# Kernel optimization log

Measured on AMD Instinct MI355X. Metric: run time of the kernel, lower is better.

## Reference

```python
import jax, jax.numpy as jnp
import numpy as np

# Grid / problem sizes (full-res grid for sp_tensor_1; sp_tensor_2 lives on the half-res grid
# and its indices are multiplied by 2 in forward, so they land on even full-res coords).
B, Z, Y, X = 2, 21, 400, 352
Z2, Y2, X2 = 11, 200, 176
N1, N2 = 160000, 60000
CIN, COUT = 64, 128
EPS = 1e-3  # BatchNorm eps


def _build_rulebook():
    """Precompute the SubMConv3d rulebook (spconv builds this once per indice_key).
    Returns padded gather/scatter index arrays for the 26 non-center taps and N.
    Padding uses index N (a dummy zero row / dropped output row)."""
    rng = np.random.default_rng(0)
    # sp_tensor_2: unique voxels on half-res grid, coords scaled by 2 (as done in forward)
    lin2 = rng.choice(B * Z2 * Y2 * X2, size=N2, replace=False)
    b2 = lin2 // (Z2 * Y2 * X2); r = lin2 % (Z2 * Y2 * X2)
    z2 = r // (Y2 * X2); r = r % (Y2 * X2); y2 = r // X2; x2 = r % X2
    c2 = np.stack([b2, 2 * z2, 2 * y2, 2 * x2], 1).astype(np.int64)
    key2 = ((c2[:, 0] * Z + c2[:, 1]) * Y + c2[:, 2]) * X + c2[:, 3]
    # sp_tensor_1: unique voxels on full-res grid, disjoint from scaled sp2 voxels
    lin1 = rng.choice(B * Z * Y * X, size=N1 + 20000, replace=False)
    lin1 = lin1[~np.isin(lin1, key2)][:N1].astype(np.int64)
    b1 = lin1 // (Z * Y * X); r = lin1 % (Z * Y * X)
    z1 = r // (Y * X); r = r % (Y * X); y1 = r // X; x1 = r % X
    c1 = np.stack([b1, z1, y1, x1], 1)
    coords = np.concatenate([c1, c2], 0)  # [N,4] -- sp1 rows first, matching feature concat
    N = coords.shape[0]
    keys = ((coords[:, 0] * Z + coords[:, 1]) * Y + coords[:, 2]) * X + coords[:, 3]
    order = np.argsort(keys); skeys = keys[order]
    gathers, scatters = [], []
    for dz in (-1, 0, 1):
        for dy in (-1, 0, 1):
            for dx in (-1, 0, 1):
                if dz == 0 and dy == 0 and dx == 0:
                    continue  # center tap handled as a dense identity-indexed GEMM
                q = coords[:, 1:] + np.array([dz, dy, dx])
                valid = (q >= 0).all(1) & (q[:, 0] < Z) & (q[:, 1] < Y) & (q[:, 2] < X)
                qk = ((coords[:, 0] * Z + q[:, 0]) * Y + q[:, 1]) * X + q[:, 2]
                pos = np.clip(np.searchsorted(skeys, qk), 0, N - 1)
                hit = valid & (skeys[pos] == qk)
                gathers.append(order[pos[hit]])
                scatters.append(np.nonzero(hit)[0])
    Pmax = max(len(g) for g in gathers)
    G = np.full((26, Pmax), N, np.int32)
    S = np.full((26, Pmax), N, np.int32)
    for i, (g, s) in enumerate(zip(gathers, scatters)):
        G[i, :len(g)] = g
        S[i, :len(s)] = s
    return G, S, N


def setup_inputs() -> dict:
    G, S, N = _build_rulebook()
    k1, k2, k3, k4 = jax.random.split(jax.random.key(0), 4)
    return {
        "features1": jax.random.normal(k1, (N1, CIN), jnp.float32),
        "features2": jax.random.normal(k2, (N - N1, CIN), jnp.float32),
        "weight": jax.random.normal(k3, (27, CIN, COUT), jnp.float32) * (1.0 / np.sqrt(27 * CIN)),
        "bias": jax.random.normal(k4, (COUT,), jnp.float32) * 0.01,
        "gamma": jnp.ones((COUT,), jnp.float32),
        "beta": jnp.zeros((COUT,), jnp.float32),
        "gather_idx": jnp.asarray(G),
        "scatter_idx": jnp.asarray(S),
    }


def reference(features1, features2, weight, bias, gamma, beta, gather_idx, scatter_idx):
    # forward(): concat features of both sparse tensors along the voxel axis
    feats = jnp.concatenate([features1, features2], axis=0)  # [N, Cin]
    N = feats.shape[0]
    # SubMConv3d via gather-GEMM-scatter over the precomputed rulebook.
    # Center tap (kernel index 13): every output voxel pairs with itself -> dense GEMM.
    out = feats @ weight[13] + bias  # [N, Cout]
    # dummy row N absorbs padded rulebook entries
    out = jnp.concatenate([out, jnp.zeros((1, out.shape[1]), out.dtype)], axis=0)
    feats_pad = jnp.concatenate([feats, jnp.zeros((1, feats.shape[1]), feats.dtype)], axis=0)
    taps = [k for k in range(27) if k != 13]
    for i, k in enumerate(taps):
        msg = feats_pad[gather_idx[i]] @ weight[k]  # [Pmax, Cout]
        out = out.at[scatter_idx[i]].add(msg)
    out = out[:N]
    # BatchNorm1d (training mode: batch statistics, biased variance) + ReLU
    mean = jnp.mean(out, axis=0)
    var = jnp.var(out, axis=0)
    out = (out - mean) * jax.lax.rsqrt(var + EPS) * gamma + beta
    return jax.nn.relu(out)
```

## Files before the change

kernel.cpp:

```cpp
#include <hip/hip_runtime.h>

#define EPS 1e-3f

typedef __attribute__((ext_vector_type(8))) short bf8_t;
typedef __attribute__((ext_vector_type(4))) float f32x4;

static __device__ __forceinline__ unsigned f2bf_pack(float a, float b) {
  union { float f; unsigned u; } ca, cb;
  ca.f = a; cb.f = b;
  unsigned ra = (ca.u + 0x7FFFu + ((ca.u >> 16) & 1u)) >> 16;
  unsigned rb = (cb.u + 0x7FFFu + ((cb.u >> 16) & 1u)) >> 16;
  return ra | (rb << 16);
}
static __device__ __forceinline__ unsigned short f2bf1(float x) {
  union { float f; unsigned u; } c; c.f = x;
  return (unsigned short)((c.u + 0x7FFFu + ((c.u >> 16) & 1u)) >> 16);
}
static __device__ __forceinline__ float bf2f(unsigned bits16) {
  union { unsigned u; float f; } c;
  c.u = bits16 << 16;
  return c.f;
}


__global__ __launch_bounds__(256) void to_bf16(
    const float* __restrict__ f1, const float* __restrict__ f2,
    unsigned short* __restrict__ fbuf, int N1, int N) {
  int idx = blockIdx.x * 256 + threadIdx.x;
  if (idx >= (N + 1) * 8) return;
  int row = idx >> 3, seg = idx & 7;
  uint4 o = make_uint4(0, 0, 0, 0);
  if (row < N) {
    const float* src = (row < N1) ? (f1 + (size_t)row * 64)
                                  : (f2 + (size_t)(row - N1) * 64);
    float4 v0 = *(const float4*)(src + seg * 8);
    float4 v1 = *(const float4*)(src + seg * 8 + 4);
    o.x = f2bf_pack(v0.x, v0.y); o.y = f2bf_pack(v0.z, v0.w);
    o.z = f2bf_pack(v1.x, v1.y); o.w = f2bf_pack(v1.z, v1.w);
  }
  *(uint4*)(fbuf + (size_t)idx * 8) = o;
}

__global__ __launch_bounds__(256) void wconv(
    const float* __restrict__ W, unsigned short* __restrict__ Wb) {
  int idx = blockIdx.x * 256 + threadIdx.x;
  int k = idx & 63, n = (idx >> 6) & 127, t = idx >> 13;
  Wb[idx] = f2bf1(W[((size_t)t * 64 + k) * 128 + n]);
}

__global__ __launch_bounds__(256) void count_slots(
    const int* __restrict__ S, unsigned char* __restrict__ SL,
    int* __restrict__ cnt, int N, int pm) {
  const int p = blockIdx.x * 256 + threadIdx.x;
  const int i = blockIdx.y;
  if (p >= pm) return;
  const int idx = i * pm + p;
  const int s = S[idx];
  if (s < N) SL[idx] = (unsigned char)atomicAdd(&cnt[s], 1);
}

__global__ __launch_bounds__(256) void prefix_base(
    const int* __restrict__ cnt, int2* __restrict__ BC,
    int* __restrict__ gtot, int N) {
  const int t = threadIdx.x;
  const int j0 = blockIdx.x * 1024 + t * 4;
  int c0 = 0, c1 = 0, c2 = 0, c3 = 0;
  if (j0 + 3 < N) {
    int4 c = *(const int4*)(cnt + j0);
    c0 = c.x; c1 = c.y; c2 = c.z; c3 = c.w;
  } else {
    if (j0 < N) c0 = cnt[j0];
    if (j0 + 1 < N) c1 = cnt[j0 + 1];
    if (j0 + 2 < N) c2 = cnt[j0 + 2];
  }
  const int tsum = c0 + c1 + c2 + c3;
  int incl = tsum;
#pragma unroll
  for (int off = 1; off < 64; off <<= 1) {
    int u = __shfl_up(incl, off, 64);
    if ((t & 63) >= off) incl += u;
  }
  __shared__ int wsum[4];
  if ((t & 63) == 63) wsum[t >> 6] = incl;
  __syncthreads();
  if (t == 0) {
    int w0 = wsum[0], w1 = wsum[1], w2 = wsum[2], w3 = wsum[3];
    int gb = atomicAdd(gtot, w0 + w1 + w2 + w3);
    wsum[0] = gb; wsum[1] = gb + w0;
    wsum[2] = gb + w0 + w1; wsum[3] = gb + w0 + w1 + w2;
  }
  __syncthreads();
  const int excl = wsum[t >> 6] + incl - tsum;
  if (j0 < N) BC[j0] = make_int2(excl, c0);
  if (j0 + 1 < N) BC[j0 + 1] = make_int2(excl + c0, c1);
  if (j0 + 2 < N) BC[j0 + 2] = make_int2(excl + c0 + c1, c2);
  if (j0 + 3 < N) BC[j0 + 3] = make_int2(excl + c0 + c1 + c2, c3);
}

__global__ __launch_bounds__(256) void center_mfma(
    const unsigned short* __restrict__ fbuf,
    const unsigned short* __restrict__ Wb13,
    const float* __restrict__ bias,
    unsigned short* __restrict__ outb, int N) {
  __shared__ unsigned short A[128 * 64];
  const int tid = threadIdx.x;
  const int row0 = blockIdx.x * 128;

#pragma unroll
  for (int it = 0; it < 4; ++it) {
    int flat = it * 256 + tid;
    int r = flat >> 3, qs = flat & 7;
    int g = row0 + r; if (g >= N) g = N;
    uint4 v = *(const uint4*)(fbuf + (size_t)g * 64 + qs * 8);
    int rt = r >> 4, m = r & 15, c = qs >> 2, qq = qs & 3;
    *(uint4*)(A + ((rt * 2 + c) * 64 + qq * 16 + m) * 8) = v;
  }
  __syncthreads();

  const int wave = tid >> 6, lane = tid & 63;
  const int ncol = lane & 15, q2 = lane >> 4;
  bf8_t Bf[2][2];
  float bs[2];
#pragma unroll
  for (int ct = 0; ct < 2; ++ct) {
    int col = wave * 32 + ct * 16 + ncol;
    bs[ct] = bias[col];
#pragma unroll
    for (int c = 0; c < 2; ++c)
      Bf[ct][c] = *(const bf8_t*)(Wb13 + (size_t)col * 64 + c * 32 + q2 * 8);
  }
  f32x4 acc[8][2];
#pragma unroll
  for (int rt = 0; rt < 8; ++rt)
#pragma unroll
    for (int ct = 0; ct < 2; ++ct) acc[rt][ct] = (f32x4){0.f, 0.f, 0.f, 0.f};

#pragma unroll
  for (int rt = 0; rt < 8; ++rt) {
    bf8_t a0 = *(const bf8_t*)(A + ((rt * 2 + 0) * 64 + lane) * 8);
    bf8_t a1 = *(const bf8_t*)(A + ((rt * 2 + 1) * 64 + lane) * 8);
#pragma unroll
    for (int ct = 0; ct < 2; ++ct) {
      acc[rt][ct] = __builtin_amdgcn_mfma_f32_16x16x32_bf16(a0, Bf[ct][0], acc[rt][ct], 0, 0, 0);
      acc[rt][ct] = __builtin_amdgcn_mfma_f32_16x16x32_bf16(a1, Bf[ct][1], acc[rt][ct], 0, 0, 0);
    }
  }

#pragma unroll
  for (int rt = 0; rt < 8; ++rt)
#pragma unroll
    for (int ct = 0; ct < 2; ++ct) {
      int col = wave * 32 + ct * 16 + ncol;
#pragma unroll
      for (int e = 0; e < 4; ++e) {
        int row = row0 + rt * 16 + q2 * 4 + e;
        if (row < N)
          outb[(size_t)row * 128 + col] = f2bf1(acc[rt][ct][e] + bs[ct]);
      }
    }
}

__global__ __launch_bounds__(256) void msg_mfma_c(
    const unsigned short* __restrict__ fbuf,
    const unsigned short* __restrict__ Wb,
    const int* __restrict__ G, const int* __restrict__ S,
    const int2* __restrict__ BC, const unsigned char* __restrict__ SL,
    unsigned short* __restrict__ compact, int N, int pm) {
  const int tap = blockIdx.y;
  const int ktap = tap + (tap >= 13 ? 1 : 0);
  const unsigned short* Wt = Wb + (size_t)ktap * 128 * 64;
  const int* Gi = G + (size_t)tap * pm;
  const int* Si = S + (size_t)tap * pm;
  const int p0 = blockIdx.x * 128;
  if (Gi[p0] >= N) return;

  __shared__ unsigned short A[128 * 64];
  __shared__ int g_lds[128];
  __shared__ int d_lds[128];
  const int tid = threadIdx.x;
  if (tid < 128) {
    int p = p0 + tid;
    int g = N, d = -1;
    if (p < pm) {
      g = Gi[p];
      int s = Si[p];
      if (s < N) d = BC[s].x + (int)SL[(size_t)tap * pm + p];
    }
    g_lds[tid] = g;
    d_lds[tid] = d;
  }
  __syncthreads();

#pragma unroll
  for (int it = 0; it < 4; ++it) {
    int flat = it * 256 + tid;
    int r = flat >> 3, qs = flat & 7;
    int g = g_lds[r];
    uint4 v = *(const uint4*)(fbuf + (size_t)g * 64 + qs * 8);
    int rt = r >> 4, m = r & 15, c = qs >> 2, qq = qs & 3;
    *(uint4*)(A + ((rt * 2 + c) * 64 + qq * 16 + m) * 8) = v;
  }
  __syncthreads();

  const int wave = tid >> 6, lane = tid & 63;
  const int ncol = lane & 15, q2 = lane >> 4;
  bf8_t Bf[2][2];
#pragma unroll
  for (int ct = 0; ct < 2; ++ct) {
    int col = wave * 32 + ct * 16 + ncol;
#pragma unroll
    for (int c = 0; c < 2; ++c)
      Bf[ct][c] = *(const bf8_t*)(Wt + (size_t)col * 64 + c * 32 + q2 * 8);
  }
  f32x4 acc[8][2];
#pragma unroll
  for (int rt = 0; rt < 8; ++rt)
#pragma unroll
    for (int ct = 0; ct < 2; ++ct) acc[rt][ct] = (f32x4){0.f, 0.f, 0.f, 0.f};

#pragma unroll
  for (int rt = 0; rt < 8; ++rt) {
    bf8_t a0 = *(const bf8_t*)(A + ((rt * 2 + 0) * 64 + lane) * 8);
    bf8_t a1 = *(const bf8_t*)(A + ((rt * 2 + 1) * 64 + lane) * 8);
#pragma unroll
    for (int ct = 0; ct < 2; ++ct) {
      acc[rt][ct] = __builtin_amdgcn_mfma_f32_16x16x32_bf16(a0, Bf[ct][0], acc[rt][ct], 0, 0, 0);
      acc[rt][ct] = __builtin_amdgcn_mfma_f32_16x16x32_bf16(a1, Bf[ct][1], acc[rt][ct], 0, 0, 0);
    }
  }

#pragma unroll
  for (int rt = 0; rt < 8; ++rt) {
    int dl[4];
#pragma unroll
    for (int e = 0; e < 4; ++e) dl[e] = d_lds[rt * 16 + q2 * 4 + e];
#pragma unroll
    for (int ct = 0; ct < 2; ++ct) {
      int col = wave * 32 + ct * 16 + ncol;
#pragma unroll
      for (int e = 0; e < 4; ++e)
        if (dl[e] >= 0)
          compact[(size_t)dl[e] * 128 + col] = f2bf1(acc[rt][ct][e]);
    }
  }
}

__global__ __launch_bounds__(256) void combine_c(
    unsigned short* __restrict__ outb, const int2* __restrict__ BC,
    const unsigned short* __restrict__ compact, float* __restrict__ ws,
    int N) {
  const int tid = threadIdx.x;
  const int grp = tid >> 5, l = tid & 31;
  float4 s = make_float4(0.f, 0.f, 0.f, 0.f);
  float4 q = make_float4(0.f, 0.f, 0.f, 0.f);

  for (int j = blockIdx.x * 8 + grp; j < N; j += gridDim.x * 8) {
    int2 bc = BC[j];
    uint2 ov = ((const uint2*)(outb + (size_t)j * 128))[l];
    float4 v;
    v.x = bf2f(ov.x & 0xffffu); v.y = bf2f(ov.x >> 16);
    v.z = bf2f(ov.y & 0xffffu); v.w = bf2f(ov.y >> 16);
    for (int k = 0; k < bc.y; ++k) {
      uint2 mv = ((const uint2*)(compact + (size_t)(bc.x + k) * 128))[l];
      v.x += bf2f(mv.x & 0xffffu); v.y += bf2f(mv.x >> 16);
      v.z += bf2f(mv.y & 0xffffu); v.w += bf2f(mv.y >> 16);
    }
    if (bc.y) {
      uint2 pk;
      pk.x = f2bf_pack(v.x, v.y); pk.y = f2bf_pack(v.z, v.w);
      ((uint2*)(outb + (size_t)j * 128))[l] = pk;
    }
    s.x += v.x; s.y += v.y; s.z += v.z; s.w += v.w;
    q.x += v.x * v.x; q.y += v.y * v.y; q.z += v.z * v.z; q.w += v.w * v.w;
  }

  __shared__ float red[8 * 32 * 9];
  float* my = red + (grp * 32 + l) * 9;
  my[0] = s.x; my[1] = s.y; my[2] = s.z; my[3] = s.w;
  my[4] = q.x; my[5] = q.y; my[6] = q.z; my[7] = q.w;
  __syncthreads();
  {
    int c4 = tid & 31, jj = tid >> 5;
    float v = 0.f;
#pragma unroll
    for (int g = 0; g < 8; ++g) v += red[(g * 32 + c4) * 9 + jj];
    int col = c4 * 4 + (jj & 3);
    unsafeAtomicAdd(&ws[(jj >> 2) * 4096 + col * 16], v);
  }
}

__global__ __launch_bounds__(256) void norm_b(
    const unsigned short* __restrict__ outb, float* __restrict__ out,
    const float* __restrict__ ws, const float* __restrict__ gamma,
    const float* __restrict__ beta, int total8, float invN) {
  const int tid0 = blockIdx.x * 256 + threadIdx.x;
  const int c0 = (tid0 & 15) * 8;
  float sc[8], sh[8];
#pragma unroll
  for (int k = 0; k < 8; ++k) {
    float m = ws[(c0 + k) * 16] * invN;
    float var = ws[4096 + (c0 + k) * 16] * invN - m * m;
    sc[k] = gamma[c0 + k] * rsqrtf(var + EPS);
    sh[k] = beta[c0 + k] - m * sc[k];
  }
  for (int idx = tid0; idx < total8; idx += gridDim.x * 256) {
    uint4 v = *(const uint4*)(outb + (size_t)idx * 8);
    float f0 = bf2f(v.x & 0xffffu), f1 = bf2f(v.x >> 16);
    float f2 = bf2f(v.y & 0xffffu), f3 = bf2f(v.y >> 16);
    float f4 = bf2f(v.z & 0xffffu), f5 = bf2f(v.z >> 16);
    float f6 = bf2f(v.w & 0xffffu), f7 = bf2f(v.w >> 16);
    float4 o0, o1;
    o0.x = fmaxf(f0 * sc[0] + sh[0], 0.f);
    o0.y = fmaxf(f1 * sc[1] + sh[1], 0.f);
    o0.z = fmaxf(f2 * sc[2] + sh[2], 0.f);
    o0.w = fmaxf(f3 * sc[3] + sh[3], 0.f);
    o1.x = fmaxf(f4 * sc[4] + sh[4], 0.f);
    o1.y = fmaxf(f5 * sc[5] + sh[5], 0.f);
    o1.z = fmaxf(f6 * sc[6] + sh[6], 0.f);
    o1.w = fmaxf(f7 * sc[7] + sh[7], 0.f);
    *(float4*)(out + (size_t)idx * 8) = o0;
    *(float4*)(out + (size_t)idx * 8 + 4) = o1;
  }
}


__global__ __launch_bounds__(256) void scatter_R(
    const int* __restrict__ S, int* __restrict__ R, int N, int pm) {
  const int p = blockIdx.x * 256 + threadIdx.x;
  const int i = blockIdx.y;
  if (p >= pm) return;
  const int idx = i * pm + p;
  const int s = S[idx];
  if (s < N) R[(size_t)s * 26 + i] = idx;
}

__global__ __launch_bounds__(256) void center_gemm(
    const float* __restrict__ f1, const float* __restrict__ f2,
    const float* __restrict__ W, const float* __restrict__ bias,
    float* __restrict__ out, int N, int N1) {
  __shared__ float fLDS[128 * 65];
  __shared__ float wLDS[32 * 128];
  const int tid = threadIdx.x;
  const int tx = tid & 15, ty = tid >> 4;
  const int row0 = blockIdx.x * 128;

  for (int k = 0; k < 8; ++k) {
    int flat4 = tid + k * 256;
    int row = flat4 >> 4, c4 = flat4 & 15;
    int grow = row0 + row;
    float4 v = make_float4(0.f, 0.f, 0.f, 0.f);
    if (grow < N) {
      const float* src = (grow < N1) ? (f1 + (size_t)grow * 64)
                                     : (f2 + (size_t)(grow - N1) * 64);
      v = *(const float4*)(src + c4 * 4);
    }
    int l = row * 65 + c4 * 4;
    fLDS[l + 0] = v.x; fLDS[l + 1] = v.y; fLDS[l + 2] = v.z; fLDS[l + 3] = v.w;
  }
  float acc[8][8];
#pragma unroll
  for (int r = 0; r < 8; ++r)
#pragma unroll
    for (int j = 0; j < 8; ++j) acc[r][j] = 0.f;
  for (int kk = 0; kk < 64; kk += 32) {
    __syncthreads();
    for (int k = 0; k < 4; ++k) {
      int flat4 = tid + k * 256;
      int c = flat4 >> 5, col4 = flat4 & 31;
      float4 v = *(const float4*)(W + (size_t)(kk + c) * 128 + col4 * 4);
      *(float4*)(wLDS + c * 128 + col4 * 4) = v;
    }
    __syncthreads();
#pragma unroll 4
    for (int c = 0; c < 32; ++c) {
      float a[8];
#pragma unroll
      for (int r = 0; r < 8; ++r) a[r] = fLDS[(ty * 8 + r) * 65 + kk + c];
      float4 b0 = *(const float4*)(wLDS + c * 128 + tx * 8);
      float4 b1 = *(const float4*)(wLDS + c * 128 + tx * 8 + 4);
      float b[8] = {b0.x, b0.y, b0.z, b0.w, b1.x, b1.y, b1.z, b1.w};
#pragma unroll
      for (int r = 0; r < 8; ++r)
#pragma unroll
        for (int j = 0; j < 8; ++j) acc[r][j] += a[r] * b[j];
    }
  }
  float4 bi0 = *(const float4*)(bias + tx * 8);
  float4 bi1 = *(const float4*)(bias + tx * 8 + 4);
#pragma unroll
  for (int r = 0; r < 8; ++r) {
    int grow = row0 + ty * 8 + r;
    if (grow < N) {
      float4 o0 = make_float4(acc[r][0] + bi0.x, acc[r][1] + bi0.y,
                              acc[r][2] + bi0.z, acc[r][3] + bi0.w);
      float4 o1 = make_float4(acc[r][4] + bi1.x, acc[r][5] + bi1.y,
                              acc[r][6] + bi1.z, acc[r][7] + bi1.w);
      float* dst = out + (size_t)grow * 128 + tx * 8;
      *(float4*)dst = o0;
      *(float4*)(dst + 4) = o1;
    }
  }
}

__global__ __launch_bounds__(256) void msg_gemm_buf(
    const float* __restrict__ f1, const float* __restrict__ f2,
    const float* __restrict__ W27, const int* __restrict__ G,
    const int* __restrict__ S, unsigned short* __restrict__ msgbuf,
    int N, int N1, int pm) {
  const int i = blockIdx.y;
  const int ktap = i + (i >= 13 ? 1 : 0);
  const float* W = W27 + (size_t)ktap * 64 * 128;
  const int* Gi = G + (size_t)i * pm;
  const int* Si = S + (size_t)i * pm;
  const int p0 = blockIdx.x * 128;
  if (Si[p0] >= N) return;
  __shared__ float fLDS[128 * 65];
  __shared__ float wLDS[32 * 128];
  const int tid = threadIdx.x;
  const int tx = tid & 15, ty = tid >> 4;
  for (int k = 0; k < 8; ++k) {
    int flat4 = tid + k * 256;
    int row = flat4 >> 4, c4 = flat4 & 15;
    int p = p0 + row;
    float4 v = make_float4(0.f, 0.f, 0.f, 0.f);
    if (p < pm) {
      int g = Gi[p];
      if (g < N) {
        const float* src = (g < N1) ? (f1 + (size_t)g * 64)
                                    : (f2 + (size_t)(g - N1) * 64);
        v = *(const float4*)(src + c4 * 4);
      }
    }
    int l = row * 65 + c4 * 4;
    fLDS[l + 0] = v.x; fLDS[l + 1] = v.y; fLDS[l + 2] = v.z; fLDS[l + 3] = v.w;
  }
  float acc[8][8];
#pragma unroll
  for (int r = 0; r < 8; ++r)
#pragma unroll
    for (int j = 0; j < 8; ++j) acc[r][j] = 0.f;
  for (int kk = 0; kk < 64; kk += 32) {
    __syncthreads();
    for (int k = 0; k < 4; ++k) {
      int flat4 = tid + k * 256;
      int c = flat4 >> 5, col4 = flat4 & 31;
      float4 v = *(const float4*)(W + (size_t)(kk + c) * 128 + col4 * 4);
      *(float4*)(wLDS + c * 128 + col4 * 4) = v;
    }
    __syncthreads();
#pragma unroll 4
    for (int c = 0; c < 32; ++c) {
      float a[8];
#pragma unroll
      for (int r = 0; r < 8; ++r) a[r] = fLDS[(ty * 8 + r) * 65 + kk + c];
      float4 b0 = *(const float4*)(wLDS + c * 128 + tx * 8);
      float4 b1 = *(const float4*)(wLDS + c * 128 + tx * 8 + 4);
      float b[8] = {b0.x, b0.y, b0.z, b0.w, b1.x, b1.y, b1.z, b1.w};
#pragma unroll
      for (int r = 0; r < 8; ++r)
#pragma unroll
        for (int j = 0; j < 8; ++j) acc[r][j] += a[r] * b[j];
    }
  }
#pragma unroll
  for (int r = 0; r < 8; ++r) {
    int p = p0 + ty * 8 + r;
    if (p < pm) {
      uint4 pk;
      pk.x = f2bf_pack(acc[r][0], acc[r][1]);
      pk.y = f2bf_pack(acc[r][2], acc[r][3]);
      pk.z = f2bf_pack(acc[r][4], acc[r][5]);
      pk.w = f2bf_pack(acc[r][6], acc[r][7]);
      *(uint4*)(msgbuf + ((size_t)i * pm + p) * 128 + tx * 8) = pk;
    }
  }
}

__global__ __launch_bounds__(256) void msg_gemm(
    const float* __restrict__ f1, const float* __restrict__ f2,
    const float* __restrict__ W27, const int* __restrict__ G,
    const int* __restrict__ S, float* __restrict__ out,
    int N, int N1, int pm) {
  const int i = blockIdx.y;
  const int ktap = i + (i >= 13 ? 1 : 0);
  const float* W = W27 + (size_t)ktap * 64 * 128;
  const int* Gi = G + (size_t)i * pm;
  const int* Si = S + (size_t)i * pm;
  const int p0 = blockIdx.x * 128;
  if (Si[p0] >= N) return;
  __shared__ float fLDS[128 * 65];
  __shared__ float wLDS[32 * 128];
  const int tid = threadIdx.x;
  const int tx = tid & 15, ty = tid >> 4;
  for (int k = 0; k < 8; ++k) {
    int flat4 = tid + k * 256;
    int row = flat4 >> 4, c4 = flat4 & 15;
    int p = p0 + row;
    float4 v = make_float4(0.f, 0.f, 0.f, 0.f);
    if (p < pm) {
      int g = Gi[p];
      if (g < N) {
        const float* src = (g < N1) ? (f1 + (size_t)g * 64)
                                    : (f2 + (size_t)(g - N1) * 64);
        v = *(const float4*)(src + c4 * 4);
      }
    }
    int l = row * 65 + c4 * 4;
    fLDS[l + 0] = v.x; fLDS[l + 1] = v.y; fLDS[l + 2] = v.z; fLDS[l + 3] = v.w;
  }
  float acc[8][8];
#pragma unroll
  for (int r = 0; r < 8; ++r)
#pragma unroll
    for (int j = 0; j < 8; ++j) acc[r][j] = 0.f;
  for (int kk = 0; kk < 64; kk += 32) {
    __syncthreads();
    for (int k = 0; k < 4; ++k) {
      int flat4 = tid + k * 256;
      int c = flat4 >> 5, col4 = flat4 & 31;
      float4 v = *(const float4*)(W + (size_t)(kk + c) * 128 + col4 * 4);
      *(float4*)(wLDS + c * 128 + col4 * 4) = v;
    }
    __syncthreads();
#pragma unroll 4
    for (int c = 0; c < 32; ++c) {
      float a[8];
#pragma unroll
      for (int r = 0; r < 8; ++r) a[r] = fLDS[(ty * 8 + r) * 65 + kk + c];
      float4 b0 = *(const float4*)(wLDS + c * 128 + tx * 8);
      float4 b1 = *(const float4*)(wLDS + c * 128 + tx * 8 + 4);
      float b[8] = {b0.x, b0.y, b0.z, b0.w, b1.x, b1.y, b1.z, b1.w};
#pragma unroll
      for (int r = 0; r < 8; ++r)
#pragma unroll
        for (int j = 0; j < 8; ++j) acc[r][j] += a[r] * b[j];
    }
  }
#pragma unroll
  for (int r = 0; r < 8; ++r) {
    int p = p0 + ty * 8 + r;
    if (p < pm) {
      int s = Si[p];
      if (s < N) {
        float* dst = out + (size_t)s * 128 + tx * 8;
#pragma unroll
        for (int j = 0; j < 8; ++j) unsafeAtomicAdd(dst + j, acc[r][j]);
      }
    }
  }
}

__global__ __launch_bounds__(256) void combine_stats(
    float* __restrict__ out, const int* __restrict__ R,
    const unsigned short* __restrict__ msgbuf, float* __restrict__ ws,
    int N) {
  const int tid = threadIdx.x;
  const int grp = tid >> 5, l = tid & 31;
  const int base = tid & 32;
  float4 s = make_float4(0.f, 0.f, 0.f, 0.f);
  float4 q = make_float4(0.f, 0.f, 0.f, 0.f);
  for (int j = blockIdx.x * 8 + grp; j < N; j += gridDim.x * 8) {
    float4 v = ((const float4*)(out + (size_t)j * 128))[l];
    int r = (l < 26) ? R[(size_t)j * 26 + l] : -1;
    unsigned long long bal = __ballot(r >= 0);
    unsigned mym = (unsigned)((bal >> base) & 0x3FFFFFFull);
    const bool any = (mym != 0);
    while (mym) {
      int b = __builtin_ctz(mym);
      mym &= mym - 1;
      int ptr = __shfl(r, base + b, 64);
      uint2 mv = ((const uint2*)(msgbuf + (size_t)ptr * 128))[l];
      v.x += bf2f(mv.x & 0xffffu);
      v.y += bf2f(mv.x >> 16);
      v.z += bf2f(mv.y & 0xffffu);
      v.w += bf2f(mv.y >> 16);
    }
    if (any) ((float4*)(out + (size_t)j * 128))[l] = v;
    s.x += v.x; s.y += v.y; s.z += v.z; s.w += v.w;
    q.x += v.x * v.x; q.y += v.y * v.y; q.z += v.z * v.z; q.w += v.w * v.w;
  }
  __shared__ float red[8 * 32 * 8];
  float* my = red + (grp * 32 + l) * 8;
  my[0] = s.x; my[1] = s.y; my[2] = s.z; my[3] = s.w;
  my[4] = q.x; my[5] = q.y; my[6] = q.z; my[7] = q.w;
  __syncthreads();
  {
    int c4 = tid & 31, j = tid >> 5;
    float v = 0.f;
#pragma unroll
    for (int g = 0; g < 8; ++g) v += red[(g * 32 + c4) * 8 + j];
    int col = c4 * 4 + (j & 3);
    unsafeAtomicAdd(&ws[col + (j >> 2) * 128], v);
  }
}

__global__ __launch_bounds__(256) void stats_kernel(
    const float* __restrict__ out, float* __restrict__ ws, int total4) {
  const int tid = threadIdx.x;
  float4 s = make_float4(0.f, 0.f, 0.f, 0.f);
  float4 q = make_float4(0.f, 0.f, 0.f, 0.f);
  const float4* o4 = (const float4*)out;
  for (int idx = blockIdx.x * 256 + tid; idx < total4; idx += gridDim.x * 256) {
    float4 v = o4[idx];
    s.x += v.x; s.y += v.y; s.z += v.z; s.w += v.w;
    q.x += v.x * v.x; q.y += v.y * v.y; q.z += v.z * v.z; q.w += v.w * v.w;
  }
  __shared__ float red[8 * 32 * 8];
  const int col4 = tid & 31, grpq = tid >> 5;
  float* my = red + (grpq * 32 + col4) * 8;
  my[0] = s.x; my[1] = s.y; my[2] = s.z; my[3] = s.w;
  my[4] = q.x; my[5] = q.y; my[6] = q.z; my[7] = q.w;
  __syncthreads();
  {
    int c4 = tid & 31, j = tid >> 5;
    float v = 0.f;
#pragma unroll
    for (int g = 0; g < 8; ++g) v += red[(g * 32 + c4) * 8 + j];
    int col = c4 * 4 + (j & 3);
    unsafeAtomicAdd(&ws[col + (j >> 2) * 128], v);
  }
}

__global__ __launch_bounds__(256) void norm_kernel(
    float* __restrict__ out, const float* __restrict__ ws,
    const float* __restrict__ gamma, const float* __restrict__ beta,
    int total4, float invN) {
  const int tid = threadIdx.x;
  const int c4 = tid & 31;
  float4 s = ((const float4*)ws)[c4];
  float4 q = ((const float4*)ws)[32 + c4];
  float4 g = ((const float4*)gamma)[c4];
  float4 b = ((const float4*)beta)[c4];
  float m0 = s.x * invN, m1 = s.y * invN, m2 = s.z * invN, m3 = s.w * invN;
  float sc0 = g.x * rsqrtf(q.x * invN - m0 * m0 + EPS);
  float sc1 = g.y * rsqrtf(q.y * invN - m1 * m1 + EPS);
  float sc2 = g.z * rsqrtf(q.z * invN - m2 * m2 + EPS);
  float sc3 = g.w * rsqrtf(q.w * invN - m3 * m3 + EPS);
  float sh0 = b.x - m0 * sc0, sh1 = b.y - m1 * sc1;
  float sh2 = b.z - m2 * sc2, sh3 = b.w - m3 * sc3;
  float4* o4 = (float4*)out;
  for (int idx = blockIdx.x * 256 + tid; idx < total4; idx += gridDim.x * 256) {
    float4 v = o4[idx];
    v.x = fmaxf(v.x * sc0 + sh0, 0.f);
    v.y = fmaxf(v.y * sc1 + sh1, 0.f);
    v.z = fmaxf(v.z * sc2 + sh2, 0.f);
    v.w = fmaxf(v.w * sc3 + sh3, 0.f);
    o4[idx] = v;
  }
}

extern "C" void kernel_launch(void* const* d_in, const int* in_sizes, int n_in,
                              void* d_out, int out_size, void* d_ws, size_t ws_size,
                              hipStream_t stream) {
  const float* f1 = (const float*)d_in[0];
  const float* f2 = (const float*)d_in[1];
  const float* W = (const float*)d_in[2];
  const float* bias = (const float*)d_in[3];
  const float* gamma = (const float*)d_in[4];
  const float* beta = (const float*)d_in[5];
  const int* G = (const int*)d_in[6];
  const int* S = (const int*)d_in[7];
  const int N1 = in_sizes[0] / 64;
  const int N2 = in_sizes[1] / 64;
  const int N = N1 + N2;
  const int pm = in_sizes[6] / 26;
  float* out = (float*)d_out;
  float* ws = (float*)d_ws;

  const size_t AL = 255;
  const size_t offC = 32768;
  const size_t Cb = (size_t)N * 4;
  const size_t offBC = (offC + Cb + AL) & ~AL;
  const size_t BCb = (size_t)N * 8;
  const size_t offSL = (offBC + BCb + AL) & ~AL;
  const size_t SLb = (size_t)26 * pm;
  const size_t offF = (offSL + SLb + AL) & ~AL;
  const size_t Fb = (size_t)(N + 1) * 64 * 2;
  const size_t offW = (offF + Fb + AL) & ~AL;
  const size_t Wbyt = (size_t)27 * 128 * 64 * 2;
  const size_t offM = (offW + Wbyt + AL) & ~AL;
  const size_t Mb = (size_t)26 * pm * 128 * 2;
  const size_t offO = (offM + Mb + AL) & ~AL;
  const size_t Ob = (size_t)N * 128 * 2;
  const bool full = ws_size >= offO + Ob;

  const size_t Rb = (size_t)N * 26 * 4;
  const size_t offR2 = 1024;
  const size_t offM2 = (offR2 + Rb + AL) & ~AL;
  const bool fast2 = ws_size >= offM2 + Mb;

  if (full) {
    int* cnt = (int*)((char*)d_ws + offC);
    int2* BC = (int2*)((char*)d_ws + offBC);
    unsigned char* SLp = (unsigned char*)((char*)d_ws + offSL);
    unsigned short* fbuf = (unsigned short*)((char*)d_ws + offF);
    unsigned short* Wb = (unsigned short*)((char*)d_ws + offW);
    unsigned short* compact = (unsigned short*)((char*)d_ws + offM);
    unsigned short* outb = (unsigned short*)((char*)d_ws + offO);
    int* gtot = (int*)((char*)d_ws + 28672);

    (void)hipMemsetAsync(ws, 0, 32768, stream);
    (void)hipMemsetAsync(cnt, 0, Cb, stream);
    to_bf16<<<((N + 1) * 8 + 255) / 256, 256, 0, stream>>>(f1, f2, fbuf, N1, N);
    wconv<<<(27 * 128 * 64) / 256, 256, 0, stream>>>(W, Wb);
    count_slots<<<dim3((pm + 255) / 256, 26), 256, 0, stream>>>(S, SLp, cnt, N, pm);
    prefix_base<<<(N + 1023) / 1024, 256, 0, stream>>>(cnt, BC, gtot, N);

    center_mfma<<<(N + 127) / 128, 256, 0, stream>>>(
        fbuf, Wb + (size_t)13 * 128 * 64, bias, outb, N);
    msg_mfma_c<<<dim3((pm + 127) / 128, 26), 256, 0, stream>>>(
        fbuf, Wb, G, S, BC, SLp, compact, N, pm);

    combine_c<<<2048, 256, 0, stream>>>(outb, BC, compact, ws, N);
    norm_b<<<2048, 256, 0, stream>>>(outb, out, ws, gamma, beta, N * 16,
                                     1.0f / N);
  } else if (fast2) {
    int* R = (int*)((char*)d_ws + offR2);
    unsigned short* msgbuf = (unsigned short*)((char*)d_ws + offM2);
    (void)hipMemsetAsync(ws, 0, 256 * sizeof(float), stream);
    (void)hipMemsetAsync(R, 0xFF, Rb, stream);
    center_gemm<<<(N + 127) / 128, 256, 0, stream>>>(
        f1, f2, W + (size_t)13 * 64 * 128, bias, out, N, N1);
    scatter_R<<<dim3((pm + 255) / 256, 26), 256, 0, stream>>>(S, R, N, pm);
    msg_gemm_buf<<<dim3((pm + 127) / 128, 26), 256, 0, stream>>>(
        f1, f2, W, G, S, msgbuf, N, N1, pm);
    combine_stats<<<1024, 256, 0, stream>>>(out, R, msgbuf, ws, N);
    norm_kernel<<<2048, 256, 0, stream>>>(out, ws, gamma, beta, N * 32,
                                          1.0f / N);
  } else {
    (void)hipMemsetAsync(ws, 0, 256 * sizeof(float), stream);
    center_gemm<<<(N + 127) / 128, 256, 0, stream>>>(
        f1, f2, W + (size_t)13 * 64 * 128, bias, out, N, N1);
    msg_gemm<<<dim3((pm + 127) / 128, 26), 256, 0, stream>>>(
        f1, f2, W, G, S, out, N, N1, pm);
    stats_kernel<<<1024, 256, 0, stream>>>(out, ws, N * 32);
    norm_kernel<<<2048, 256, 0, stream>>>(out, ws, gamma, beta, N * 32,
                                          1.0f / N);
  }
}
```

Baseline: 334.1 us.

## Fuse prep kernels and merge center GEMM into combine/stats pass

Merges the bf16 feature conversion, weight conversion and slot-counting kernels into one launch, and folds the two memsets into a single contiguous memset. Moves the center-tap MFMA GEMM into the combine kernel, so the center result stays in LDS and is summed with the compacted messages before the single write of outb. This removes one full round-trip of the bf16 output tensor plus several launch gaps. The combine kernel now uses 32KB of LDS and a fixed 128-row block tiling instead of a grid-stride loop, which may lower occupancy and load balance.

Result: faster. 297.1 us (-11.1%).

```diff
diff --git a/kernel.cpp b/kernel.cpp
--- a/kernel.cpp
+++ b/kernel.cpp
@@ -23,40 +23,41 @@
 }
 
 
-__global__ __launch_bounds__(256) void to_bf16(
+__global__ __launch_bounds__(256) void prep(
+    const float* __restrict__ W, unsigned short* __restrict__ Wb,
     const float* __restrict__ f1, const float* __restrict__ f2,
-    unsigned short* __restrict__ fbuf, int N1, int N) {
-  int idx = blockIdx.x * 256 + threadIdx.x;
-  if (idx >= (N + 1) * 8) return;
-  int row = idx >> 3, seg = idx & 7;
-  uint4 o = make_uint4(0, 0, 0, 0);
-  if (row < N) {
-    const float* src = (row < N1) ? (f1 + (size_t)row * 64)
-                                  : (f2 + (size_t)(row - N1) * 64);
-    float4 v0 = *(const float4*)(src + seg * 8);
-    float4 v1 = *(const float4*)(src + seg * 8 + 4);
-    o.x = f2bf_pack(v0.x, v0.y); o.y = f2bf_pack(v0.z, v0.w);
-    o.z = f2bf_pack(v1.x, v1.y); o.w = f2bf_pack(v1.z, v1.w);
-  }
-  *(uint4*)(fbuf + (size_t)idx * 8) = o;
-}
-
-__global__ __launch_bounds__(256) void wconv(
-    const float* __restrict__ W, unsigned short* __restrict__ Wb) {
-  int idx = blockIdx.x * 256 + threadIdx.x;
-  int k = idx & 63, n = (idx >> 6) & 127, t = idx >> 13;
-  Wb[idx] = f2bf1(W[((size_t)t * 64 + k) * 128 + n]);
-}
-
-__global__ __launch_bounds__(256) void count_slots(
+    unsigned short* __restrict__ fbuf,
     const int* __restrict__ S, unsigned char* __restrict__ SL,
-    int* __restrict__ cnt, int N, int pm) {
-  const int p = blockIdx.x * 256 + threadIdx.x;
-  const int i = blockIdx.y;
-  if (p >= pm) return;
-  const int idx = i * pm + p;
-  const int s = S[idx];
-  if (s < N) SL[idx] = (unsigned char)atomicAdd(&cnt[s], 1);
+    int* __restrict__ cnt, int N, int N1, int pm,
+    int wblocks, int fblocks, int cpb) {
+  const int bid = blockIdx.x;
+  if (bid < wblocks) {
+    int idx = bid * 256 + threadIdx.x;
+    int k = idx & 63, n = (idx >> 6) & 127, t = idx >> 13;
+    Wb[idx] = f2bf1(W[((size_t)t * 64 + k) * 128 + n]);
+  } else if (bid < wblocks + fblocks) {
+    int idx = (bid - wblocks) * 256 + threadIdx.x;
+    if (idx >= (N + 1) * 8) return;
+    int row = idx >> 3, seg = idx & 7;
+    uint4 o = make_uint4(0, 0, 0, 0);
+    if (row < N) {
+      const float* src = (row < N1) ? (f1 + (size_t)row * 64)
+                                    : (f2 + (size_t)(row - N1) * 64);
+      float4 v0 = *(const float4*)(src + seg * 8);
+      float4 v1 = *(const float4*)(src + seg * 8 + 4);
+      o.x = f2bf_pack(v0.x, v0.y); o.y = f2bf_pack(v0.z, v0.w);
+      o.z = f2bf_pack(v1.x, v1.y); o.w = f2bf_pack(v1.z, v1.w);
+    }
+    *(uint4*)(fbuf + (size_t)idx * 8) = o;
+  } else {
+    int b = bid - wblocks - fblocks;
+    int tap = b / cpb;
+    int p = (b - tap * cpb) * 256 + threadIdx.x;
+    if (p >= pm) return;
+    const int idx = tap * pm + p;
+    const int s = S[idx];
+    if (s < N) SL[idx] = (unsigned char)atomicAdd(&cnt[s], 1);
+  }
 }
 
 __global__ __launch_bounds__(256) void prefix_base(
@@ -97,69 +98,6 @@
   if (j0 + 3 < N) BC[j0 + 3] = make_int2(excl + c0 + c1 + c2, c3);
 }
 
-__global__ __launch_bounds__(256) void center_mfma(
-    const unsigned short* __restrict__ fbuf,
-    const unsigned short* __restrict__ Wb13,
-    const float* __restrict__ bias,
-    unsigned short* __restrict__ outb, int N) {
-  __shared__ unsigned short A[128 * 64];
-  const int tid = threadIdx.x;
-  const int row0 = blockIdx.x * 128;
-
-#pragma unroll
-  for (int it = 0; it < 4; ++it) {
-    int flat = it * 256 + tid;
-    int r = flat >> 3, qs = flat & 7;
-    int g = row0 + r; if (g >= N) g = N;
-    uint4 v = *(const uint4*)(fbuf + (size_t)g * 64 + qs * 8);
-    int rt = r >> 4, m = r & 15, c = qs >> 2, qq = qs & 3;
-    *(uint4*)(A + ((rt * 2 + c) * 64 + qq * 16 + m) * 8) = v;
-  }
-  __syncthreads();
-
-  const int wave = tid >> 6, lane = tid & 63;
-  const int ncol = lane & 15, q2 = lane >> 4;
-  bf8_t Bf[2][2];
-  float bs[2];
-#pragma unroll
-  for (int ct = 0; ct < 2; ++ct) {
-    int col = wave * 32 + ct * 16 + ncol;
-    bs[ct] = bias[col];
-#pragma unroll
-    for (int c = 0; c < 2; ++c)
-      Bf[ct][c] = *(const bf8_t*)(Wb13 + (size_t)col * 64 + c * 32 + q2 * 8);
-  }
-  f32x4 acc[8][2];
-#pragma unroll
-  for (int rt = 0; rt < 8; ++rt)
-#pragma unroll
-    for (int ct = 0; ct < 2; ++ct) acc[rt][ct] = (f32x4){0.f, 0.f, 0.f, 0.f};
-
-#pragma unroll
-  for (int rt = 0; rt < 8; ++rt) {
-    bf8_t a0 = *(const bf8_t*)(A + ((rt * 2 + 0) * 64 + lane) * 8);
-    bf8_t a1 = *(const bf8_t*)(A + ((rt * 2 + 1) * 64 + lane) * 8);
-#pragma unroll
-    for (int ct = 0; ct < 2; ++ct) {
-      acc[rt][ct] = __builtin_amdgcn_mfma_f32_16x16x32_bf16(a0, Bf[ct][0], acc[rt][ct], 0, 0, 0);
-      acc[rt][ct] = __builtin_amdgcn_mfma_f32_16x16x32_bf16(a1, Bf[ct][1], acc[rt][ct], 0, 0, 0);
-    }
-  }
-
-#pragma unroll
-  for (int rt = 0; rt < 8; ++rt)
-#pragma unroll
-    for (int ct = 0; ct < 2; ++ct) {
-      int col = wave * 32 + ct * 16 + ncol;
-#pragma unroll
-      for (int e = 0; e < 4; ++e) {
-        int row = row0 + rt * 16 + q2 * 4 + e;
-        if (row < N)
-          outb[(size_t)row * 128 + col] = f2bf1(acc[rt][ct][e] + bs[ct]);
-      }
-    }
-}
-
 __global__ __launch_bounds__(256) void msg_mfma_c(
     const unsigned short* __restrict__ fbuf,
     const unsigned short* __restrict__ Wb,
@@ -245,36 +183,100 @@
   }
 }
 
-__global__ __launch_bounds__(256) void combine_c(
-    unsigned short* __restrict__ outb, const int2* __restrict__ BC,
-    const unsigned short* __restrict__ compact, float* __restrict__ ws,
-    int N) {
+__global__ __launch_bounds__(256) void center_combine(
+    const unsigned short* __restrict__ fbuf,
+    const unsigned short* __restrict__ Wb13, const float* __restrict__ bias,
+    const int2* __restrict__ BC, const unsigned short* __restrict__ compact,
+    unsigned short* __restrict__ outb, float* __restrict__ ws, int N) {
+  __shared__ unsigned short SH[128 * 128];
+  __shared__ int2 bc_lds[128];
   const int tid = threadIdx.x;
+  const int row0 = blockIdx.x * 128;
+
+  if (tid < 128) {
+    int j = row0 + tid;
+    bc_lds[tid] = (j < N) ? BC[j] : make_int2(0, 0);
+  }
+
+#pragma unroll
+  for (int it = 0; it < 4; ++it) {
+    int flat = it * 256 + tid;
+    int r = flat >> 3, qs = flat & 7;
+    int g = row0 + r; if (g >= N) g = N;
+    uint4 v = *(const uint4*)(fbuf + (size_t)g * 64 + qs * 8);
+    int rt = r >> 4, m = r & 15, c = qs >> 2, qq = qs & 3;
+    *(uint4*)(SH + ((rt * 2 + c) * 64 + qq * 16 + m) * 8) = v;
+  }
+  __syncthreads();
+
+  const int wave = tid >> 6, lane = tid & 63;
+  const int ncol = lane & 15, q2 = lane >> 4;
+  bf8_t Bf[2][2];
+  float bs[2];
+#pragma unroll
+  for (int ct = 0; ct < 2; ++ct) {
+    int col = wave * 32 + ct * 16 + ncol;
+    bs[ct] = bias[col];
+#pragma unroll
+    for (int c = 0; c < 2; ++c)
+      Bf[ct][c] = *(const bf8_t*)(Wb13 + (size_t)col * 64 + c * 32 + q2 * 8);
+  }
+  f32x4 acc[8][2];
+#pragma unroll
+  for (int rt = 0; rt < 8; ++rt)
+#pragma unroll
+    for (int ct = 0; ct < 2; ++ct) acc[rt][ct] = (f32x4){0.f, 0.f, 0.f, 0.f};
+
+#pragma unroll
+  for (int rt = 0; rt < 8; ++rt) {
+    bf8_t a0 = *(const bf8_t*)(SH + ((rt * 2 + 0) * 64 + lane) * 8);
+    bf8_t a1 = *(const bf8_t*)(SH + ((rt * 2 + 1) * 64 + lane) * 8);
+#pragma unroll
+    for (int ct = 0; ct < 2; ++ct) {
+      acc[rt][ct] = __builtin_amdgcn_mfma_f32_16x16x32_bf16(a0, Bf[ct][0], acc[rt][ct], 0, 0, 0);
+      acc[rt][ct] = __builtin_amdgcn_mfma_f32_16x16x32_bf16(a1, Bf[ct][1], acc[rt][ct], 0, 0, 0);
+    }
+  }
+  __syncthreads();
+
+#pragma unroll
+  for (int rt = 0; rt < 8; ++rt)
+#pragma unroll
+    for (int ct = 0; ct < 2; ++ct) {
+      int col = wave * 32 + ct * 16 + ncol;
+#pragma unroll
+      for (int e = 0; e < 4; ++e)
+        SH[(rt * 16 + q2 * 4 + e) * 128 + col] = f2bf1(acc[rt][ct][e] + bs[ct]);
+    }
+  __syncthreads();
+
   const int grp = tid >> 5, l = tid & 31;
   float4 s = make_float4(0.f, 0.f, 0.f, 0.f);
   float4 q = make_float4(0.f, 0.f, 0.f, 0.f);
-
-  for (int j = blockIdx.x * 8 + grp; j < N; j += gridDim.x * 8) {
-    int2 bc = BC[j];
-    uint2 ov = ((const uint2*)(outb + (size_t)j * 128))[l];
+#pragma unroll 1
+  for (int i = 0; i < 16; ++i) {
+    int r = grp * 16 + i;
+    int j = row0 + r;
+    if (j >= N) break;
+    int2 bc = bc_lds[r];
+    uint2 cv = ((const uint2*)(SH + r * 128))[l];
     float4 v;
-    v.x = bf2f(ov.x & 0xffffu); v.y = bf2f(ov.x >> 16);
-    v.z = bf2f(ov.y & 0xffffu); v.w = bf2f(ov.y >> 16);
+    v.x = bf2f(cv.x & 0xffffu); v.y = bf2f(cv.x >> 16);
+    v.z = bf2f(cv.y & 0xffffu); v.w = bf2f(cv.y >> 16);
     for (int k = 0; k < bc.y; ++k) {
       uint2 mv = ((const uint2*)(compact + (size_t)(bc.x + k) * 128))[l];
       v.x += bf2f(mv.x & 0xffffu); v.y += bf2f(mv.x >> 16);
       v.z += bf2f(mv.y & 0xffffu); v.w += bf2f(mv.y >> 16);
     }
-    if (bc.y) {
-      uint2 pk;
-      pk.x = f2bf_pack(v.x, v.y); pk.y = f2bf_pack(v.z, v.w);
-      ((uint2*)(outb + (size_t)j * 128))[l] = pk;
-    }
+    uint2 pk;
+    pk.x = f2bf_pack(v.x, v.y); pk.y = f2bf_pack(v.z, v.w);
+    ((uint2*)(outb + (size_t)j * 128))[l] = pk;
     s.x += v.x; s.y += v.y; s.z += v.z; s.w += v.w;
     q.x += v.x * v.x; q.y += v.y * v.y; q.z += v.z * v.z; q.w += v.w * v.w;
   }
 
-  __shared__ float red[8 * 32 * 9];
+  __syncthreads();
+  float* red = (float*)SH;
   float* my = red + (grp * 32 + l) * 9;
   my[0] = s.x; my[1] = s.y; my[2] = s.z; my[3] = s.w;
   my[4] = q.x; my[5] = q.y; my[6] = q.z; my[7] = q.w;
@@ -699,19 +701,21 @@
     unsigned short* outb = (unsigned short*)((char*)d_ws + offO);
     int* gtot = (int*)((char*)d_ws + 28672);
 
-    (void)hipMemsetAsync(ws, 0, 32768, stream);
-    (void)hipMemsetAsync(cnt, 0, Cb, stream);
-    to_bf16<<<((N + 1) * 8 + 255) / 256, 256, 0, stream>>>(f1, f2, fbuf, N1, N);
-    wconv<<<(27 * 128 * 64) / 256, 256, 0, stream>>>(W, Wb);
-    count_slots<<<dim3((pm + 255) / 256, 26), 256, 0, stream>>>(S, SLp, cnt, N, pm);
+    const int wblocks = (27 * 128 * 64) / 256;
+    const int fblocks = ((N + 1) * 8 + 255) / 256;
+    const int cpb256 = (pm + 255) / 256;
+    const int cpb128 = (pm + 127) / 128;
+    const int cblocks = (N + 127) / 128;
+
+    (void)hipMemsetAsync(ws, 0, offC + Cb, stream);
+    prep<<<wblocks + fblocks + 26 * cpb256, 256, 0, stream>>>(
+        W, Wb, f1, f2, fbuf, S, SLp, cnt, N, N1, pm, wblocks, fblocks,
+        cpb256);
     prefix_base<<<(N + 1023) / 1024, 256, 0, stream>>>(cnt, BC, gtot, N);
-
-    center_mfma<<<(N + 127) / 128, 256, 0, stream>>>(
-        fbuf, Wb + (size_t)13 * 128 * 64, bias, outb, N);
-    msg_mfma_c<<<dim3((pm + 127) / 128, 26), 256, 0, stream>>>(
+    msg_mfma_c<<<dim3(cpb128, 26), 256, 0, stream>>>(
         fbuf, Wb, G, S, BC, SLp, compact, N, pm);
-
-    combine_c<<<2048, 256, 0, stream>>>(outb, BC, compact, ws, N);
+    center_combine<<<cblocks, 256, 0, stream>>>(
+        fbuf, Wb + (size_t)13 * 128 * 64, bias, BC, compact, outb, ws, N);
     norm_b<<<2048, 256, 0, stream>>>(outb, out, ws, gamma, beta, N * 16,
                                      1.0f / N);
   } else if (fast2) {
```
